# Kernel tuning notes

Measured on AMD Instinct MI355X. Metric: run time of the kernel, lower is better.

## Reference

```python
import jax, jax.numpy as jnp
import numpy as np

N = 2048  # nodes; num_node_features == N per __init__
E = 65536 # directed edges (avg degree 32)
H1, H2 = 32, 20


def setup_inputs() -> dict:
    key = jax.random.key(0)
    ks = jax.random.split(key, 10)
    u = lambda k, shape, fan: jax.random.uniform(k, shape, jnp.float32, -1.0, 1.0) / np.sqrt(fan)
    x = jax.random.normal(ks[0], (N, N), jnp.float32)
    edge_index = jax.random.randint(ks[1], (2, E), 0, N, jnp.int64)
    return {
        'x': x,
        'edge_index': edge_index,
        'W1': u(ks[2], (N, H1), N),   'b1': u(ks[3], (H1,), N),
        'W2': u(ks[4], (H1, H2), H1), 'b2': u(ks[5], (H2,), H1),
        'aW': u(ks[6], (H2, N * N), H2), 'ab': u(ks[7], (N * N,), H2),
        'cW': u(ks[8], (H2, 1), H2),  'cb': u(ks[9], (1,), H2),
    }


def gcn_conv(x, edge_index, W, b):
    # GCNConv: D^{-1/2} (A + I) D^{-1/2} X W + b, aggregated at target nodes
    loop = jnp.arange(N)
    src = jnp.concatenate([edge_index[0], loop])
    dst = jnp.concatenate([edge_index[1], loop])
    deg = jax.ops.segment_sum(jnp.ones_like(dst, dtype=x.dtype), dst, num_segments=N)
    dinv = jnp.where(deg > 0, jax.lax.rsqrt(deg), 0.0)
    norm = dinv[src] * dinv[dst]                      # [E+N]
    h = x @ W                                         # [N, out]
    msg = h[src] * norm[:, None]                      # gather + scale
    return jax.ops.segment_sum(msg, dst, num_segments=N) + b


def reference(x, edge_index, W1, b1, W2, b2, aW, ab, cW, cb):
    h = jax.nn.relu(gcn_conv(x, edge_index, W1, b1))
    h = jax.nn.relu(gcn_conv(h, edge_index, W2, b2))
    critic_output = (h @ cW + cb).mean(axis=0)        # [1]
    x_actor = h.mean(axis=0)                          # [20]
    logits = (x_actor @ aW + ab).reshape(N, N)
    probs = jax.nn.softmax(logits, axis=1)
    flat = probs.reshape(-1)
    # Faithful replication of the sequential two-max scan: the second 'max'
    # is the running max just before the final update, i.e. the argmax of the
    # prefix strictly before the global argmax (0,0 if argmax is at flat[0]).
    idx1 = jnp.argmax(flat)
    masked = jnp.where(jnp.arange(N * N) < idx1, flat, -jnp.inf)
    idx2 = jnp.argmax(masked)  # argmax over all -inf -> 0, matching (si,sj)=(0,0)
    actions = jnp.stack([
        jnp.stack([idx1 // N, idx1 % N]),
        jnp.stack([idx2 // N, idx2 % N]),
    ])  # [2, 2] int
    # Faithful to original: indexes the FLATTENED probs with the (i,j) pairs
    log_probs = -jnp.log(flat[actions])               # [2, 2]
    return actions, log_probs, critic_output
```

## Files before the change

### kernel.cpp

```cpp
#include <hip/hip_runtime.h>
#include <hip/hip_bf16.h>
#include <math.h>

#define NN_NODES 2048
#define NE 65536
#define H1C 32
#define H2C 20
#define AW_STRIDE 4194304ull

__global__ void k_deg(const int* __restrict__ ei, int* __restrict__ deg) {
    int e = blockIdx.x * 256 + threadIdx.x;
    if (e < NE) atomicAdd(&deg[ei[NE + e]], 1);
}

__global__ void k_scan(const int* __restrict__ deg, float* __restrict__ dinv,
                       int* __restrict__ off) {
    __shared__ int s[1024];
    int t = threadIdx.x;
    int d0 = deg[2 * t], d1 = deg[2 * t + 1];
    dinv[2 * t]     = rsqrtf((float)(d0 + 1));
    dinv[2 * t + 1] = rsqrtf((float)(d1 + 1));
    s[t] = d0 + d1;
    __syncthreads();
    for (int o = 1; o < 1024; o <<= 1) {
        int add = (t >= o) ? s[t - o] : 0;
        __syncthreads();
        s[t] += add;
        __syncthreads();
    }
    int excl = (t > 0) ? s[t - 1] : 0;
    off[2 * t] = excl;
    off[2 * t + 1] = excl + d0;
    if (t == 1023) off[2048] = s[1023];
}

__global__ void k_scatter(const int* __restrict__ ei, const float* __restrict__ dinv,
                          const int* __restrict__ off, int* __restrict__ cnt,
                          int* __restrict__ csr_src, float* __restrict__ csr_norm) {
    int e = blockIdx.x * 256 + threadIdx.x;
    if (e >= NE) return;
    int s = ei[e], d = ei[NE + e];
    int pos = off[d] + atomicAdd(&cnt[d], 1);
    csr_src[pos] = s;
    csr_norm[pos] = dinv[s] * dinv[d];
}

__global__ __launch_bounds__(256) void k_gemm1(const float* __restrict__ X,
                                               const float* __restrict__ W1,
                                               float* __restrict__ h_tmp) {
    __shared__ float Xs[32][33];
    __shared__ __align__(16) float Ws[32][32];
    int t = threadIdx.x;
    int rg = blockIdx.x >> 3, kc = blockIdx.x & 7;
    int r0 = rg * 32;
    int r = t >> 3, c4 = (t & 7) * 4;
    float4 acc = {0.f, 0.f, 0.f, 0.f};
    for (int kt = 0; kt < 8; ++kt) {
        int k0 = kc * 256 + kt * 32;
#pragma unroll
        for (int i = 0; i < 4; ++i) {
            int id = t + i * 256;
            int rr = id >> 5, kk = id & 31;
            Xs[rr][kk] = X[(size_t)(r0 + rr) * 2048 + k0 + kk];
            Ws[rr][kk] = W1[(size_t)(k0 + rr) * 32 + kk];
        }
        __syncthreads();
#pragma unroll
        for (int kk = 0; kk < 32; ++kk) {
            float a = Xs[r][kk];
            float4 b = *(const float4*)&Ws[kk][c4];
            acc.x += a * b.x; acc.y += a * b.y; acc.z += a * b.z; acc.w += a * b.w;
        }
        __syncthreads();
    }
    float* dst = &h_tmp[(size_t)(r0 + r) * 32 + c4];
    atomicAdd(dst + 0, acc.x);
    atomicAdd(dst + 1, acc.y);
    atomicAdd(dst + 2, acc.z);
    atomicAdd(dst + 3, acc.w);
}

template <int C>
__global__ __launch_bounds__(256) void k_agg(const float* __restrict__ h,
                                             const float* __restrict__ csr_norm,
                                             const int* __restrict__ csr_src,
                                             const int* __restrict__ off,
                                             const float* __restrict__ dinv,
                                             const float* __restrict__ bias,
                                             float* __restrict__ out) {
    int n = blockIdx.x;
    int t = threadIdx.x;
    int c = t & 31, s = t >> 5;
    __shared__ float red[8][32];
    float acc = 0.f;
    int e0 = off[n], e1 = off[n + 1];
    if (c < C) {
        for (int e = e0 + s; e < e1; e += 8) {
            int src = csr_src[e];
            acc += h[(size_t)src * C + c] * csr_norm[e];
        }
    }
    red[s][c] = acc;
    __syncthreads();
    if (t < 32) {
        float v = red[0][t];
#pragma unroll
        for (int i = 1; i < 8; ++i) v += red[i][t];
        if (t < C) {
            float dn = dinv[n];
            v += h[(size_t)n * C + t] * dn * dn + bias[t];
            out[(size_t)n * C + t] = fmaxf(v, 0.f);
        }
    }
}

__global__ __launch_bounds__(256) void k_gemm2(const float* __restrict__ h1,
                                               const float* __restrict__ W2,
                                               float* __restrict__ h2t) {
    __shared__ float Ws[H1C * H2C];
    int t = threadIdx.x;
    for (int i = t; i < H1C * H2C; i += 256) Ws[i] = W2[i];
    __syncthreads();
    int id = blockIdx.x * 256 + t;
    int n = id / 20, c = id % 20;
    const float* hr = &h1[(size_t)n * 32];
    float acc = 0.f;
#pragma unroll
    for (int k = 0; k < 32; ++k) acc += hr[k] * Ws[k * 20 + c];
    h2t[(size_t)n * 20 + c] = acc;
}

__global__ __launch_bounds__(640) void k_xa(const float* __restrict__ h2,
                                            float* __restrict__ xa_sum) {
    __shared__ float red[640];
    int t = threadIdx.x;
    int nl = t / 20, c = t % 20;
    int n = blockIdx.x * 32 + nl;
    red[t] = h2[(size_t)n * 20 + c];
    __syncthreads();
    for (int o = 16; o >= 1; o >>= 1) {
        if (nl < o) red[t] += red[(nl + o) * 20 + c];
        __syncthreads();
    }
    if (t < 20) atomicAdd(&xa_sum[t], red[t]);
}

__global__ __launch_bounds__(256) void k_rows(const float* __restrict__ aW,
                                              const float* __restrict__ ab,
                                              const float* __restrict__ xa_sum,
                                              float* __restrict__ rowM,
                                              float* __restrict__ rowZ,
                                              int* __restrict__ rowC) {
    __shared__ float xa[20];
    __shared__ float redf[256];
    __shared__ int redi[256];
    int t = threadIdx.x;
    int row = blockIdx.x;
    if (t < 20) xa[t] = xa_sum[t] * (1.0f / 2048.0f);
    __syncthreads();
    size_t base = (size_t)row * 2048;
    float l[8];
#pragma unroll
    for (int u = 0; u < 2; ++u) {
        int j0 = u * 1024 + t * 4;
        float4 acc = *(const float4*)&ab[base + j0];
#pragma unroll
        for (int k = 0; k < 20; ++k) {
            float4 w = *(const float4*)&aW[(size_t)k * AW_STRIDE + base + j0];
            float sv = xa[k];
            acc.x += sv * w.x; acc.y += sv * w.y; acc.z += sv * w.z; acc.w += sv * w.w;
        }
        l[u * 4 + 0] = acc.x; l[u * 4 + 1] = acc.y;
        l[u * 4 + 2] = acc.z; l[u * 4 + 3] = acc.w;
    }
    float m = l[0];
    int mi = t * 4;
#pragma unroll
    for (int q = 1; q < 8; ++q) {
        int col = (q >> 2) * 1024 + t * 4 + (q & 3);
        if (l[q] > m) { m = l[q]; mi = col; }
    }
    redf[t] = m; redi[t] = mi;
    __syncthreads();
    for (int o = 128; o >= 1; o >>= 1) {
        if (t < o) {
            float vo = redf[t + o]; int io = redi[t + o];
            if (vo > redf[t] || (vo == redf[t] && io < redi[t])) { redf[t] = vo; redi[t] = io; }
        }
        __syncthreads();
    }
    float M = redf[0];
    int C1 = redi[0];
    __syncthreads();
    float zsum = 0.f;
#pragma unroll
    for (int q = 0; q < 8; ++q) zsum += expf(l[q] - M);
    redf[t] = zsum;
    __syncthreads();
    for (int o = 128; o >= 1; o >>= 1) {
        if (t < o) redf[t] += redf[t + o];
        __syncthreads();
    }
    if (t == 0) { rowM[row] = M; rowZ[row] = redf[0]; rowC[row] = C1; }
}

__global__ __launch_bounds__(256) void k_final(const float* __restrict__ rowM,
                                               const float* __restrict__ rowZ,
                                               const int* __restrict__ rowC,
                                               const float* __restrict__ aW,
                                               const float* __restrict__ ab,
                                               const float* __restrict__ xa_sum,
                                               const float* __restrict__ cW,
                                               const float* __restrict__ cb,
                                               float* __restrict__ out) {
    __shared__ float xa[20];
    __shared__ float rf[256];
    __shared__ int ri[256];
    __shared__ float sM1, sZ1;
    __shared__ int sR1, sC1, sR2, sC2;
    int t = threadIdx.x;
    if (t < 20) xa[t] = xa_sum[t] * (1.0f / 2048.0f);
    __syncthreads();

    float z = INFINITY; int zi = 0x7fffffff;
    for (int i = t; i < 2048; i += 256) {
        float v = rowZ[i];
        if (v < z || (v == z && i < zi)) { z = v; zi = i; }
    }
    rf[t] = z; ri[t] = zi;
    __syncthreads();
    for (int o = 128; o >= 1; o >>= 1) {
        if (t < o) {
            float vo = rf[t + o]; int io = ri[t + o];
            if (vo < rf[t] || (vo == rf[t] && io < ri[t])) { rf[t] = vo; ri[t] = io; }
        }
        __syncthreads();
    }
    if (t == 0) {
        sR1 = ri[0]; sC1 = rowC[ri[0]]; sM1 = rowM[ri[0]]; sZ1 = rowZ[ri[0]];
    }
    __syncthreads();
    int r1 = sR1, c1 = sC1;

    z = INFINITY; zi = 0x7fffffff;
    for (int i = t; i < r1; i += 256) {
        float v = rowZ[i];
        if (v < z || (v == z && i < zi)) { z = v; zi = i; }
    }
    __syncthreads();
    rf[t] = z; ri[t] = zi;
    __syncthreads();
    for (int o = 128; o >= 1; o >>= 1) {
        if (t < o) {
            float vo = rf[t + o]; int io = ri[t + o];
            if (vo < rf[t] || (vo == rf[t] && io < ri[t])) { rf[t] = vo; ri[t] = io; }
        }
        __syncthreads();
    }
    float ZP = rf[0]; int iP = ri[0];
    __syncthreads();

    float lm = -INFINITY; int lj = 0x7fffffff;
    size_t base = (size_t)r1 * 2048;
    for (int j = t; j < c1; j += 256) {
        float acc = ab[base + j];
#pragma unroll
        for (int k = 0; k < 20; ++k) acc += xa[k] * aW[(size_t)k * AW_STRIDE + base + j];
        if (acc > lm) { lm = acc; lj = j; }
    }
    rf[t] = lm; ri[t] = lj;
    __syncthreads();
    for (int o = 128; o >= 1; o >>= 1) {
        if (t < o) {
            float vo = rf[t + o]; int io = ri[t + o];
            if (vo > rf[t] || (vo == rf[t] && io < ri[t])) { rf[t] = vo; ri[t] = io; }
        }
        __syncthreads();
    }
    float LB = rf[0]; int jB = ri[0];
    __syncthreads();

    if (t == 0) {
        int r2, c2;
        if (r1 == 0 && c1 == 0) {
            r2 = 0; c2 = 0;
        } else {
            bool hasA = (r1 > 0), hasB = (c1 > 0);
            float pA = hasA ? 1.0f / ZP : -INFINITY;
            float pB = hasB ? expf(LB - sM1) / sZ1 : -INFINITY;
            if (hasB && (!hasA || pB > pA)) { r2 = r1; c2 = jB; }
            else                            { r2 = iP; c2 = rowC[iP]; }
        }
        sR2 = r2; sC2 = c2;
        out[0] = (float)r1; out[1] = (float)c1;
        out[2] = (float)r2; out[3] = (float)c2;
        float cr = 0.f;
#pragma unroll
        for (int k = 0; k < 20; ++k) cr += xa[k] * cW[k];
        out[8] = cr + cb[0];
    }
    __syncthreads();

    if (t < 4) {
        int a = (t == 0) ? sR1 : (t == 1) ? sC1 : (t == 2) ? sR2 : sC2;
        float acc = ab[a];
#pragma unroll
        for (int k = 0; k < 20; ++k) acc += xa[k] * aW[(size_t)k * AW_STRIDE + a];
        float lp = (acc - rowM[0]) - logf(rowZ[0]);
        out[4 + t] = -lp;
    }
}

extern "C" void kernel_launch(void* const* d_in, const int* in_sizes, int n_in,
                              void* d_out, int out_size, void* d_ws, size_t ws_size,
                              hipStream_t stream) {
    const float* x  = (const float*)d_in[0];
    const int*   ei = (const int*)d_in[1];
    const float* W1 = (const float*)d_in[2];
    const float* b1 = (const float*)d_in[3];
    const float* W2 = (const float*)d_in[4];
    const float* b2 = (const float*)d_in[5];
    const float* aW = (const float*)d_in[6];
    const float* ab = (const float*)d_in[7];
    const float* cW = (const float*)d_in[8];
    const float* cb = (const float*)d_in[9];
    float* out = (float*)d_out;

    char* p = (char*)d_ws;
    auto alloc = [&](size_t bytes) {
        void* r = (void*)p;
        p += (bytes + 255) & ~(size_t)255;
        return r;
    };
    int*   deg    = (int*)alloc(2048 * 4);
    int*   cnt    = (int*)alloc(2048 * 4);
    float* xa_sum = (float*)alloc(64 * 4);
    float* h_tmp  = (float*)alloc(65536 * 4);
    size_t zero_bytes = (size_t)(p - (char*)d_ws);
    float* dinv     = (float*)alloc(2048 * 4);
    int*   csr_off  = (int*)alloc(2049 * 4);
    int*   csr_src  = (int*)alloc(65536 * 4);
    float* csr_norm = (float*)alloc(65536 * 4);
    float* h1       = (float*)alloc(65536 * 4);
    float* h2t      = (float*)alloc(40960 * 4);
    float* h2       = (float*)alloc(40960 * 4);
    float* rowM     = (float*)alloc(2048 * 4);
    float* rowZ     = (float*)alloc(2048 * 4);
    int*   rowC     = (int*)alloc(2048 * 4);

    hipMemsetAsync(d_ws, 0, zero_bytes, stream);
    k_deg<<<NE / 256, 256, 0, stream>>>(ei, deg);
    k_scan<<<1, 1024, 0, stream>>>(deg, dinv, csr_off);
    k_scatter<<<NE / 256, 256, 0, stream>>>(ei, dinv, csr_off, cnt, csr_src, csr_norm);
    k_gemm1<<<512, 256, 0, stream>>>(x, W1, h_tmp);
    k_agg<32><<<2048, 256, 0, stream>>>(h_tmp, csr_norm, csr_src, csr_off, dinv, b1, h1);
    k_gemm2<<<160, 256, 0, stream>>>(h1, W2, h2t);
    k_agg<20><<<2048, 256, 0, stream>>>(h2t, csr_norm, csr_src, csr_off, dinv, b2, h2);
    k_xa<<<64, 640, 0, stream>>>(h2, xa_sum);
    k_rows<<<2048, 256, 0, stream>>>(aW, ab, xa_sum, rowM, rowZ, rowC);
    k_final<<<1, 256, 0, stream>>>(rowM, rowZ, rowC, aW, ab, xa_sum, cW, cb, out);
}
```

Before: 544.8 us.

## Fuse GEMM2 and mean-pool into aggregation kernels, precompute prefix argmax per row

Folds the second dense layer into the first aggregation kernel and the node mean into the second aggregation kernel, accumulating into 32 slots with atomics. This removes the k_gemm2 and k_xa launches and the h1/h2 buffers. Zeroing of the scratch buffers moves from a large memset into k_deg, leaving only the deg memset. k_rows now also records each row's prefix max and its column, so k_final no longer runs a serial single-block pass over one row of the 20x4M aW matrix. The cost is an extra reduction in every k_rows block and more atomics in k_agg2.

```diff
diff --git a/kernel.cpp b/kernel.cpp
--- a/kernel.cpp
+++ b/kernel.cpp
@@ -8,9 +8,14 @@
 #define H2C 20
 #define AW_STRIDE 4194304ull
 
-__global__ void k_deg(const int* __restrict__ ei, int* __restrict__ deg) {
+__global__ void k_deg(const int* __restrict__ ei, int* __restrict__ deg,
+                      int* __restrict__ cnt, float* __restrict__ xa_slots,
+                      float* __restrict__ h_tmp) {
     int e = blockIdx.x * 256 + threadIdx.x;
-    if (e < NE) atomicAdd(&deg[ei[NE + e]], 1);
+    h_tmp[e] = 0.f;
+    if (e < 2048) cnt[e] = 0;
+    if (e < 640) xa_slots[e] = 0.f;
+    atomicAdd(&deg[ei[NE + e]], 1);
 }
 
 __global__ void k_scan(const int* __restrict__ deg, float* __restrict__ dinv,
@@ -80,83 +85,97 @@
     atomicAdd(dst + 3, acc.w);
 }
 
-template <int C>
-__global__ __launch_bounds__(256) void k_agg(const float* __restrict__ h,
-                                             const float* __restrict__ csr_norm,
-                                             const int* __restrict__ csr_src,
-                                             const int* __restrict__ off,
-                                             const float* __restrict__ dinv,
-                                             const float* __restrict__ bias,
-                                             float* __restrict__ out) {
+__global__ __launch_bounds__(256) void k_agg1(const float* __restrict__ h,
+                                              const float* __restrict__ csr_norm,
+                                              const int* __restrict__ csr_src,
+                                              const int* __restrict__ off,
+                                              const float* __restrict__ dinv,
+                                              const float* __restrict__ b1,
+                                              const float* __restrict__ W2,
+                                              float* __restrict__ h2t) {
+    __shared__ float W2s[H1C * H2C];
+    __shared__ float red[8][32];
+    __shared__ float hrow[32];
     int n = blockIdx.x;
     int t = threadIdx.x;
+    for (int i = t; i < H1C * H2C; i += 256) W2s[i] = W2[i];
     int c = t & 31, s = t >> 5;
-    __shared__ float red[8][32];
     float acc = 0.f;
     int e0 = off[n], e1 = off[n + 1];
-    if (c < C) {
+    for (int e = e0 + s; e < e1; e += 8) {
+        int src = csr_src[e];
+        acc += h[(size_t)src * 32 + c] * csr_norm[e];
+    }
+    red[s][c] = acc;
+    __syncthreads();
+    if (t < 32) {
+        float v = red[0][t];
+#pragma unroll
+        for (int i = 1; i < 8; ++i) v += red[i][t];
+        float dn = dinv[n];
+        v += h[(size_t)n * 32 + t] * dn * dn + b1[t];
+        hrow[t] = fmaxf(v, 0.f);
+    }
+    __syncthreads();
+    if (t < H2C) {
+        float a = 0.f;
+#pragma unroll
+        for (int k = 0; k < H1C; ++k) a += hrow[k] * W2s[k * H2C + t];
+        h2t[(size_t)n * H2C + t] = a;
+    }
+}
+
+__global__ __launch_bounds__(256) void k_agg2(const float* __restrict__ h2t,
+                                              const float* __restrict__ csr_norm,
+                                              const int* __restrict__ csr_src,
+                                              const int* __restrict__ off,
+                                              const float* __restrict__ dinv,
+                                              const float* __restrict__ b2,
+                                              float* __restrict__ xa_slots) {
+    __shared__ float red[8][32];
+    int n = blockIdx.x;
+    int t = threadIdx.x;
+    int c = t & 31, s = t >> 5;
+    float acc = 0.f;
+    int e0 = off[n], e1 = off[n + 1];
+    if (c < H2C) {
         for (int e = e0 + s; e < e1; e += 8) {
             int src = csr_src[e];
-            acc += h[(size_t)src * C + c] * csr_norm[e];
+            acc += h2t[(size_t)src * H2C + c] * csr_norm[e];
         }
     }
     red[s][c] = acc;
     __syncthreads();
-    if (t < 32) {
+    if (t < H2C) {
         float v = red[0][t];
 #pragma unroll
         for (int i = 1; i < 8; ++i) v += red[i][t];
-        if (t < C) {
-            float dn = dinv[n];
-            v += h[(size_t)n * C + t] * dn * dn + bias[t];
-            out[(size_t)n * C + t] = fmaxf(v, 0.f);
-        }
-    }
-}
-
-__global__ __launch_bounds__(256) void k_gemm2(const float* __restrict__ h1,
-                                               const float* __restrict__ W2,
-                                               float* __restrict__ h2t) {
-    __shared__ float Ws[H1C * H2C];
-    int t = threadIdx.x;
-    for (int i = t; i < H1C * H2C; i += 256) Ws[i] = W2[i];
-    __syncthreads();
-    int id = blockIdx.x * 256 + t;
-    int n = id / 20, c = id % 20;
-    const float* hr = &h1[(size_t)n * 32];
-    float acc = 0.f;
-#pragma unroll
-    for (int k = 0; k < 32; ++k) acc += hr[k] * Ws[k * 20 + c];
-    h2t[(size_t)n * 20 + c] = acc;
-}
-
-__global__ __launch_bounds__(640) void k_xa(const float* __restrict__ h2,
-                                            float* __restrict__ xa_sum) {
-    __shared__ float red[640];
-    int t = threadIdx.x;
-    int nl = t / 20, c = t % 20;
-    int n = blockIdx.x * 32 + nl;
-    red[t] = h2[(size_t)n * 20 + c];
-    __syncthreads();
-    for (int o = 16; o >= 1; o >>= 1) {
-        if (nl < o) red[t] += red[(nl + o) * 20 + c];
-        __syncthreads();
-    }
-    if (t < 20) atomicAdd(&xa_sum[t], red[t]);
+        float dn = dinv[n];
+        v += h2t[(size_t)n * H2C + t] * dn * dn + b2[t];
+        v = fmaxf(v, 0.f);
+        atomicAdd(&xa_slots[(n & 31) * H2C + t], v);
+    }
 }
 
 __global__ __launch_bounds__(256) void k_rows(const float* __restrict__ aW,
                                               const float* __restrict__ ab,
-                                              const float* __restrict__ xa_sum,
+                                              const float* __restrict__ xa_slots,
                                               float* __restrict__ rowM,
                                               float* __restrict__ rowZ,
-                                              int* __restrict__ rowC) {
+                                              int* __restrict__ rowC,
+                                              float* __restrict__ rowPM,
+                                              int* __restrict__ rowPC) {
     __shared__ float xa[20];
     __shared__ float redf[256];
     __shared__ int redi[256];
     int t = threadIdx.x;
     int row = blockIdx.x;
-    if (t < 20) xa[t] = xa_sum[t] * (1.0f / 2048.0f);
+    if (t < 20) {
+        float s = 0.f;
+#pragma unroll
+        for (int i = 0; i < 32; ++i) s += xa_slots[i * 20 + t];
+        xa[t] = s * (1.0f / 2048.0f);
+    }
     __syncthreads();
     size_t base = (size_t)row * 2048;
     float l[8];
@@ -201,15 +220,37 @@
         if (t < o) redf[t] += redf[t + o];
         __syncthreads();
     }
-    if (t == 0) { rowM[row] = M; rowZ[row] = redf[0]; rowC[row] = C1; }
+    float Z = redf[0];
+    __syncthreads();
+    float pm = -INFINITY; int pj = 0x7fffffff;
+#pragma unroll
+    for (int q = 0; q < 8; ++q) {
+        int col = (q >> 2) * 1024 + t * 4 + (q & 3);
+        if (col < C1 && l[q] > pm) { pm = l[q]; pj = col; }
+    }
+    redf[t] = pm; redi[t] = pj;
+    __syncthreads();
+    for (int o = 128; o >= 1; o >>= 1) {
+        if (t < o) {
+            float vo = redf[t + o]; int io = redi[t + o];
+            if (vo > redf[t] || (vo == redf[t] && io < redi[t])) { redf[t] = vo; redi[t] = io; }
+        }
+        __syncthreads();
+    }
+    if (t == 0) {
+        rowM[row] = M; rowZ[row] = Z; rowC[row] = C1;
+        rowPM[row] = redf[0]; rowPC[row] = redi[0];
+    }
 }
 
 __global__ __launch_bounds__(256) void k_final(const float* __restrict__ rowM,
                                                const float* __restrict__ rowZ,
                                                const int* __restrict__ rowC,
+                                               const float* __restrict__ rowPM,
+                                               const int* __restrict__ rowPC,
                                                const float* __restrict__ aW,
                                                const float* __restrict__ ab,
-                                               const float* __restrict__ xa_sum,
+                                               const float* __restrict__ xa_slots,
                                                const float* __restrict__ cW,
                                                const float* __restrict__ cb,
                                                float* __restrict__ out) {
@@ -219,7 +260,12 @@
     __shared__ float sM1, sZ1;
     __shared__ int sR1, sC1, sR2, sC2;
     int t = threadIdx.x;
-    if (t < 20) xa[t] = xa_sum[t] * (1.0f / 2048.0f);
+    if (t < 20) {
+        float s = 0.f;
+#pragma unroll
+        for (int i = 0; i < 32; ++i) s += xa_slots[i * 20 + t];
+        xa[t] = s * (1.0f / 2048.0f);
+    }
     __syncthreads();
 
     float z = INFINITY; int zi = 0x7fffffff;
@@ -258,26 +304,6 @@
         __syncthreads();
     }
     float ZP = rf[0]; int iP = ri[0];
-    __syncthreads();
-
-    float lm = -INFINITY; int lj = 0x7fffffff;
-    size_t base = (size_t)r1 * 2048;
-    for (int j = t; j < c1; j += 256) {
-        float acc = ab[base + j];
-#pragma unroll
-        for (int k = 0; k < 20; ++k) acc += xa[k] * aW[(size_t)k * AW_STRIDE + base + j];
-        if (acc > lm) { lm = acc; lj = j; }
-    }
-    rf[t] = lm; ri[t] = lj;
-    __syncthreads();
-    for (int o = 128; o >= 1; o >>= 1) {
-        if (t < o) {
-            float vo = rf[t + o]; int io = ri[t + o];
-            if (vo > rf[t] || (vo == rf[t] && io < ri[t])) { rf[t] = vo; ri[t] = io; }
-        }
-        __syncthreads();
-    }
-    float LB = rf[0]; int jB = ri[0];
     __syncthreads();
 
     if (t == 0) {
@@ -287,8 +313,8 @@
         } else {
             bool hasA = (r1 > 0), hasB = (c1 > 0);
             float pA = hasA ? 1.0f / ZP : -INFINITY;
-            float pB = hasB ? expf(LB - sM1) / sZ1 : -INFINITY;
-            if (hasB && (!hasA || pB > pA)) { r2 = r1; c2 = jB; }
+            float pB = hasB ? expf(rowPM[r1] - sM1) / sZ1 : -INFINITY;
+            if (hasB && (!hasA || pB > pA)) { r2 = r1; c2 = rowPC[r1]; }
             else                            { r2 = iP; c2 = rowC[iP]; }
         }
         sR2 = r2; sC2 = c2;
@@ -332,31 +358,28 @@
         p += (bytes + 255) & ~(size_t)255;
         return r;
     };
-    int*   deg    = (int*)alloc(2048 * 4);
-    int*   cnt    = (int*)alloc(2048 * 4);
-    float* xa_sum = (float*)alloc(64 * 4);
-    float* h_tmp  = (float*)alloc(65536 * 4);
-    size_t zero_bytes = (size_t)(p - (char*)d_ws);
+    int*   deg      = (int*)alloc(2048 * 4);
+    int*   cnt      = (int*)alloc(2048 * 4);
+    float* xa_slots = (float*)alloc(640 * 4);
+    float* h_tmp    = (float*)alloc(65536 * 4);
     float* dinv     = (float*)alloc(2048 * 4);
     int*   csr_off  = (int*)alloc(2049 * 4);
     int*   csr_src  = (int*)alloc(65536 * 4);
     float* csr_norm = (float*)alloc(65536 * 4);
-    float* h1       = (float*)alloc(65536 * 4);
     float* h2t      = (float*)alloc(40960 * 4);
-    float* h2       = (float*)alloc(40960 * 4);
     float* rowM     = (float*)alloc(2048 * 4);
     float* rowZ     = (float*)alloc(2048 * 4);
     int*   rowC     = (int*)alloc(2048 * 4);
-
-    hipMemsetAsync(d_ws, 0, zero_bytes, stream);
-    k_deg<<<NE / 256, 256, 0, stream>>>(ei, deg);
+    float* rowPM    = (float*)alloc(2048 * 4);
+    int*   rowPC    = (int*)alloc(2048 * 4);
+
+    hipMemsetAsync(deg, 0, 2048 * 4, stream);
+    k_deg<<<NE / 256, 256, 0, stream>>>(ei, deg, cnt, xa_slots, h_tmp);
     k_scan<<<1, 1024, 0, stream>>>(deg, dinv, csr_off);
     k_scatter<<<NE / 256, 256, 0, stream>>>(ei, dinv, csr_off, cnt, csr_src, csr_norm);
     k_gemm1<<<512, 256, 0, stream>>>(x, W1, h_tmp);
-    k_agg<32><<<2048, 256, 0, stream>>>(h_tmp, csr_norm, csr_src, csr_off, dinv, b1, h1);
-    k_gemm2<<<160, 256, 0, stream>>>(h1, W2, h2t);
-    k_agg<20><<<2048, 256, 0, stream>>>(h2t, csr_norm, csr_src, csr_off, dinv, b2, h2);
-    k_xa<<<64, 640, 0, stream>>>(h2, xa_sum);
-    k_rows<<<2048, 256, 0, stream>>>(aW, ab, xa_sum, rowM, rowZ, rowC);
-    k_final<<<1, 256, 0, stream>>>(rowM, rowZ, rowC, aW, ab, xa_sum, cW, cb, out);
-}
+    k_agg1<<<2048, 256, 0, stream>>>(h_tmp, csr_norm, csr_src, csr_off, dinv, b1, W2, h2t);
+    k_agg2<<<2048, 256, 0, stream>>>(h2t, csr_norm, csr_src, csr_off, dinv, b2, xa_slots);
+    k_rows<<<2048, 256, 0, stream>>>(aW, ab, xa_slots, rowM, rowZ, rowC, rowPM, rowPC);
+    k_final<<<1, 256, 0, stream>>>(rowM, rowZ, rowC, rowPM, rowPC, aW, ab, xa_slots, cW, cb, out);
+}
```

Result: no change. 541.8 us (-0.5%).
